# Kernel optimization log

Measured on AMD Instinct MI355X. Metric: run time of the kernel, lower is better.

Reference implementation:

```python
import jax, jax.numpy as jnp
import numpy as np
from jax import lax

# config (matches init_kwargs)
HEADS = 4
KD2 = 256          # key_dim // 2
KNN = 16
BLOCK = 128        # knn * block_rate
COL = 512          # value_size // block
VALUE_SIZE = 65536 # key_num ** 2
D_OUT = 512
D_IN = 1024
QUERYDIM = HEADS * KD2  # 1024
KERNEL = 3


def setup_inputs() -> dict:
    key = jax.random.key(0)
    ks = jax.random.split(key, 8)
    B, T = 2, 2048
    return {
        "x": jax.random.normal(ks[0], (B, T, D_IN), dtype=jnp.float32),
        "conv_w": jax.random.normal(ks[1], (D_IN, 1, KERNEL), dtype=jnp.float32) * 0.1,
        "conv_b": jax.random.normal(ks[2], (D_IN,), dtype=jnp.float32) * 0.1,
        "lin_w": jax.random.normal(ks[3], (QUERYDIM, D_IN), dtype=jnp.float32) * (D_IN ** -0.5),
        "lin_b": jax.random.normal(ks[4], (QUERYDIM,), dtype=jnp.float32) * 0.1,
        "rowkeys": jax.random.normal(ks[5], (BLOCK, HEADS, KD2), dtype=jnp.float32) * (KD2 ** -0.5),
        "colkeys": jax.random.normal(ks[6], (COL, HEADS, KD2), dtype=jnp.float32) * (KD2 ** -0.5),
        "value_w": jax.random.normal(ks[7], (VALUE_SIZE, D_OUT), dtype=jnp.float32),
    }


def _forward(x, conv_w, conv_b, lin_w, lin_b, rowkeys, colkeys, value_w):
    B, T, C = x.shape
    # --- Querynet: causal depthwise conv1d + linear ---
    xt = jnp.transpose(x, (0, 2, 1))  # (B, C, T)
    y = lax.conv_general_dilated(
        xt, conv_w, window_strides=(1,), padding=[(KERNEL - 1, 0)],
        feature_group_count=C, dimension_numbers=("NCH", "OIH", "NCH"))
    y = y + conv_b[None, :, None]
    y = jnp.transpose(y, (0, 2, 1))                     # (B, T, C)
    query = y @ lin_w.T + lin_b                         # (B, T, querydim)
    # torch: query.view(B, heads, T, key_dim//2) -- raw C-order reshape
    q = query.reshape(B, HEADS, T, KD2)
    # --- block_wise_choice.get_indices ---
    score = jnp.einsum("bhtd,ehd->bhte", q, rowkeys)    # (B,H,T,block)
    col_scores = jnp.einsum("bhtd,chd->bhtc", q, colkeys)  # (B,H,T,col)
    score_col, idx_col = lax.top_k(col_scores, 1)       # (B,H,T,1)
    base = jnp.arange(BLOCK, dtype=jnp.int32)
    indices = base[None, None, None, :] * COL + idx_col  # (B,H,T,block)
    score = score + score_col                            # broadcast add
    # torch .view(B,H,-1,T): raw C-order reshape mixing tokens and blocks
    score = score.reshape(B, HEADS, BLOCK, T)
    indices = indices.reshape(B, HEADS, BLOCK, T)
    k = T * KNN // BLOCK
    score_top, dispatch = lax.top_k(score, k)            # (B,H,block,k), sorted desc
    idx_top = jnp.take_along_axis(indices, dispatch, axis=-1)
    score_r = score_top.reshape(B, BLOCK, -1)            # (B, block, H*k)
    idx_r = idx_top.reshape(B, BLOCK, -1)
    disp_r = dispatch.reshape(B, BLOCK, -1)
    # --- Memory_value: gather-weight-scatter ---
    gathered = value_w[idx_r]                            # (B, block, H*k, d)
    weighted = (gathered * score_r[..., None]).reshape(B, -1, D_OUT)
    flat_disp = disp_r.reshape(B, -1)                    # values in [0, T)
    out = jnp.zeros((B, T, D_OUT), dtype=weighted.dtype)
    out = out.at[jnp.arange(B)[:, None], flat_disp].add(weighted)
    return out


def reference(x, conv_w, conv_b, lin_w, lin_b, rowkeys, colkeys, value_w):
    return _forward(x, conv_w, conv_b, lin_w, lin_b, rowkeys, colkeys, value_w)
```

## Files before the change

kernel.cpp:

```cpp
#include <hip/hip_runtime.h>

constexpr int Bc   = 2;
constexpr int Tc   = 2048;
constexpr int Cc   = 1024;
constexpr int QDc  = 1024;
constexpr int Hc   = 4;
constexpr int KD2c = 256;
constexpr int BLKc = 128;
constexpr int COLc = 512;
constexpr int DOUTc= 512;
constexpr int KSELc= 256;
constexpr int NKEYS= BLKc + COLc;
constexpr int NBINS= Bc * Tc;
constexpr int NSEL = Bc * Hc * BLKc * KSELc;

typedef short bf16x8 __attribute__((ext_vector_type(8)));
typedef float f32x4  __attribute__((ext_vector_type(4)));

__device__ __forceinline__ unsigned short f2bf(float f) {
    unsigned u = __float_as_uint(f);
    u += 0x7FFFu + ((u >> 16) & 1u);
    return (unsigned short)(u >> 16);
}
__device__ __forceinline__ float bf2f(unsigned short h) {
    return __uint_as_float((unsigned)h << 16);
}
__device__ __forceinline__ void splitbf3(float f, unsigned short* h,
                                         unsigned short* m, unsigned short* l) {
    unsigned short hh = f2bf(f);
    float r1 = f - bf2f(hh);
    unsigned short mm = f2bf(r1);
    float r2 = r1 - bf2f(mm);
    *h = hh; *m = mm; *l = f2bf(r2);
}

__device__ __forceinline__ void gld_lds16(const void* g, void* l) {
    __builtin_amdgcn_global_load_lds(
        (const __attribute__((address_space(1))) unsigned int*)g,
        (__attribute__((address_space(3))) unsigned int*)l, 16, 0, 0);
}

__global__ __launch_bounds__(256) void conv_kernel(
    const float* __restrict__ x, const float* __restrict__ cw,
    const float* __restrict__ cb, unsigned short* __restrict__ y1,
    unsigned short* __restrict__ y2, unsigned short* __restrict__ y3)
{
    int idx = blockIdx.x * 256 + threadIdx.x;
    int c = idx & (Cc - 1);
    int t = (idx >> 10) & (Tc - 1);
    int b = idx >> 21;
    float w0 = cw[c*3+0], w1 = cw[c*3+1], w2 = cw[c*3+2];
    const float* xb = x + (size_t)b * Tc * Cc;
    float acc = cb[c] + w2 * xb[(size_t)t*Cc + c];
    if (t >= 1) acc += w1 * xb[(size_t)(t-1)*Cc + c];
    if (t >= 2) acc += w0 * xb[(size_t)(t-2)*Cc + c];
    splitbf3(acc, &y1[idx], &y2[idx], &y3[idx]);
}

__global__ __launch_bounds__(256) void convw_kernel(
    const float* __restrict__ w, unsigned short* __restrict__ w1,
    unsigned short* __restrict__ w2, unsigned short* __restrict__ w3)
{
    int idx = blockIdx.x * 256 + threadIdx.x;
    splitbf3(w[idx], &w1[idx], &w2[idx], &w3[idx]);
}

__global__ __launch_bounds__(256) void convkeys_kernel(
    const float* __restrict__ rowkeys, const float* __restrict__ colkeys,
    unsigned short* __restrict__ k1, unsigned short* __restrict__ k2,
    unsigned short* __restrict__ k3)
{
    int bid = blockIdx.x;
    int h = bid / NKEYS, n = bid % NKEYS;
    int k = threadIdx.x;
    float v = (n < BLKc) ? rowkeys[((size_t)n*Hc + h)*KD2c + k]
                         : colkeys[((size_t)(n-BLKc)*Hc + h)*KD2c + k];
    size_t o = ((size_t)h*NKEYS + n)*KD2c + k;
    splitbf3(v, &k1[o], &k2[o], &k3[o]);
}

__device__ __forceinline__ void mfma_gemm_tile(
    const unsigned short* __restrict__ A1g, const unsigned short* __restrict__ A2g,
    const unsigned short* __restrict__ A3g, int lda,
    const unsigned short* __restrict__ B1g, const unsigned short* __restrict__ B2g,
    const unsigned short* __restrict__ B3g, int ldb,
    int K, int m0, int n0, char* lds, f32x4 acc[4][4])
{
    const int tid  = threadIdx.x;
    const int wave = tid >> 6, lane = tid & 63;
    const int wr = wave >> 1, wc = wave & 1;
    const int g = lane >> 4, r16 = lane & 15;

    int aoff[4], boff[4];
    #pragma unroll
    for (int i = 0; i < 4; i++) {
        int ra = wr*64 + i*16 + r16;
        aoff[i] = ra*64 + ((g ^ ((ra>>1)&3)) << 4);
        int rb = wc*64 + i*16 + r16;
        boff[i] = rb*64 + ((g ^ ((rb>>1)&3)) << 4);
    }
    const int c0 = wave*64 + lane;
    const int c1 = 256 + c0;
    const int row0 = c0 >> 2, kg0 = ((c0 & 3) ^ ((row0>>1)&3)) * 8;
    const int row1 = c1 >> 2, kg1 = ((c1 & 3) ^ ((row1>>1)&3)) * 8;
    char* d0 = lds + wave*1024;
    char* d1 = lds + 4096 + wave*1024;

    for (int kc = 0; kc < K; kc += 32) {
        size_t a0 = (size_t)(m0+row0)*lda + kc + kg0;
        size_t a1s = (size_t)(m0+row1)*lda + kc + kg1;
        size_t b0 = (size_t)(n0+row0)*ldb + kc + kg0;
        size_t b1s = (size_t)(n0+row1)*ldb + kc + kg1;
        gld_lds16(A1g + a0,  d0);
        gld_lds16(A1g + a1s, d1);
        gld_lds16(A2g + a0,  d0 + 8192);
        gld_lds16(A2g + a1s, d1 + 8192);
        gld_lds16(A3g + a0,  d0 + 16384);
        gld_lds16(A3g + a1s, d1 + 16384);
        gld_lds16(B1g + b0,  d0 + 24576);
        gld_lds16(B1g + b1s, d1 + 24576);
        gld_lds16(B2g + b0,  d0 + 32768);
        gld_lds16(B2g + b1s, d1 + 32768);
        gld_lds16(B3g + b0,  d0 + 40960);
        gld_lds16(B3g + b1s, d1 + 40960);
        __syncthreads();

        bf16x8 a1[4], a2[4], a3[4], b1[4], b2[4], b3[4];
        #pragma unroll
        for (int i = 0; i < 4; i++) {
            a1[i] = *(const bf16x8*)(lds + aoff[i]);
            a2[i] = *(const bf16x8*)(lds +  8192 + aoff[i]);
            a3[i] = *(const bf16x8*)(lds + 16384 + aoff[i]);
            b1[i] = *(const bf16x8*)(lds + 24576 + boff[i]);
            b2[i] = *(const bf16x8*)(lds + 32768 + boff[i]);
            b3[i] = *(const bf16x8*)(lds + 40960 + boff[i]);
        }
        #pragma unroll
        for (int i = 0; i < 4; i++)
            #pragma unroll
            for (int j = 0; j < 4; j++) {
                acc[i][j] = __builtin_amdgcn_mfma_f32_16x16x32_bf16(a3[i], b1[j], acc[i][j], 0, 0, 0);
                acc[i][j] = __builtin_amdgcn_mfma_f32_16x16x32_bf16(a2[i], b2[j], acc[i][j], 0, 0, 0);
                acc[i][j] = __builtin_amdgcn_mfma_f32_16x16x32_bf16(a1[i], b3[j], acc[i][j], 0, 0, 0);
                acc[i][j] = __builtin_amdgcn_mfma_f32_16x16x32_bf16(a2[i], b1[j], acc[i][j], 0, 0, 0);
                acc[i][j] = __builtin_amdgcn_mfma_f32_16x16x32_bf16(a1[i], b2[j], acc[i][j], 0, 0, 0);
                acc[i][j] = __builtin_amdgcn_mfma_f32_16x16x32_bf16(a1[i], b1[j], acc[i][j], 0, 0, 0);
            }
        __syncthreads();
    }
}

__global__ __launch_bounds__(256) void qgemm_kernel(
    const unsigned short* __restrict__ y1, const unsigned short* __restrict__ y2,
    const unsigned short* __restrict__ y3,
    const unsigned short* __restrict__ w1, const unsigned short* __restrict__ w2,
    const unsigned short* __restrict__ w3,
    const float* __restrict__ bias,
    unsigned short* __restrict__ q1, unsigned short* __restrict__ q2,
    unsigned short* __restrict__ q3)
{
    __shared__ char lds[49152];
    int m0 = blockIdx.y * 128, n0 = blockIdx.x * 128;
    f32x4 acc[4][4];
    #pragma unroll
    for (int i = 0; i < 4; i++)
        #pragma unroll
        for (int j = 0; j < 4; j++) acc[i][j] = (f32x4)0.f;
    mfma_gemm_tile(y1, y2, y3, Cc, w1, w2, w3, Cc, Cc, m0, n0, lds, acc);

    const int lane = threadIdx.x & 63, wave = threadIdx.x >> 6;
    const int wr = wave >> 1, wc = wave & 1;
    const int g = lane >> 4, r16 = lane & 15;
    #pragma unroll
    for (int i = 0; i < 4; i++)
        #pragma unroll
        for (int j = 0; j < 4; j++)
            #pragma unroll
            for (int reg = 0; reg < 4; reg++) {
                int m = m0 + wr*64 + i*16 + g*4 + reg;
                int n = n0 + wc*64 + j*16 + r16;
                float v = acc[i][j][reg] + bias[n];
                size_t o = (size_t)m * QDc + n;
                splitbf3(v, &q1[o], &q2[o], &q3[o]);
            }
}

__global__ __launch_bounds__(256) void sgemm_kernel(
    const unsigned short* __restrict__ q1, const unsigned short* __restrict__ q2,
    const unsigned short* __restrict__ q3,
    const unsigned short* __restrict__ k1, const unsigned short* __restrict__ k2,
    const unsigned short* __restrict__ k3,
    float* __restrict__ Ctmp)
{
    __shared__ char lds[49152];
    int b4h = blockIdx.z;
    size_t qo = (size_t)b4h * (Tc * KD2c);
    size_t ko = (size_t)(b4h & 3) * (NKEYS * KD2c);
    int m0 = blockIdx.y * 128, n0 = blockIdx.x * 128;
    f32x4 acc[4][4];
    #pragma unroll
    for (int i = 0; i < 4; i++)
        #pragma unroll
        for (int j = 0; j < 4; j++) acc[i][j] = (f32x4)0.f;
    mfma_gemm_tile(q1+qo, q2+qo, q3+qo, KD2c, k1+ko, k2+ko, k3+ko, KD2c,
                   KD2c, m0, n0, lds, acc);

    const int lane = threadIdx.x & 63, wave = threadIdx.x >> 6;
    const int wr = wave >> 1, wc = wave & 1;
    const int g = lane >> 4, r16 = lane & 15;
    float* Cb = Ctmp + (size_t)b4h * Tc * NKEYS;
    #pragma unroll
    for (int i = 0; i < 4; i++)
        #pragma unroll
        for (int j = 0; j < 4; j++)
            #pragma unroll
            for (int reg = 0; reg < 4; reg++) {
                int m = m0 + wr*64 + i*16 + g*4 + reg;
                int n = n0 + wc*64 + j*16 + r16;
                Cb[(size_t)m * NKEYS + n] = acc[i][j][reg];
            }
}

__global__ __launch_bounds__(256) void colmax_kernel(
    const float* __restrict__ Ctmp, float* __restrict__ s, int* __restrict__ cidx)
{
    int rid = blockIdx.x * 4 + (threadIdx.x >> 6);
    int lane = threadIdx.x & 63;
    const float* row = Ctmp + (size_t)rid * NKEYS;
    float best = -3.4e38f; int bi = 0;
    #pragma unroll
    for (int i = 0; i < 8; i++) {
        int c = lane + i*64;
        float v = row[BLKc + c];
        if (v > best) { best = v; bi = c; }
    }
    #pragma unroll
    for (int off = 32; off > 0; off >>= 1) {
        float ov = __shfl_xor(best, off, 64);
        int   oi = __shfl_xor(bi,   off, 64);
        if (ov > best || (ov == best && oi < bi)) { best = ov; bi = oi; }
    }
    if (lane == 0) cidx[rid] = bi;
    #pragma unroll
    for (int e = lane; e < BLKc; e += 64)
        s[(size_t)rid*BLKc + e] = row[e] + best;
}

__global__ __launch_bounds__(256) void topk_kernel(
    const float* __restrict__ s, const int* __restrict__ cidx,
    int* __restrict__ tk_j, int* __restrict__ tk_vidx, float* __restrict__ tk_score)
{
    int wid  = (blockIdx.x << 2) + (threadIdx.x >> 6);
    int lane = threadIdx.x & 63;
    int batch = wid >> 7;
    int i = wid & 127;
    const float* srow = s + (size_t)batch * (Tc*BLKc) + (size_t)i * 2048;

    unsigned key[8][4];
    #pragma unroll
    for (int r = 0; r < 8; r++) {
        float4 v4 = *(const float4*)&srow[r*256 + lane*4];
        float vv[4] = {v4.x, v4.y, v4.z, v4.w};
        #pragma unroll
        for (int e = 0; e < 4; e++) {
            unsigned u = __float_as_uint(vv[e]);
            key[r][e] = (u >> 31) ? ~u : (u | 0x80000000u);
        }
    }

    unsigned lo = 0, hi = 0xFFFFFFFFu;
    while (lo < hi) {
        unsigned d = hi - lo;
        unsigned mid = lo + ((d >> 1) + (d & 1u));
        int cnt = 0;
        #pragma unroll
        for (int r = 0; r < 8; r++)
            #pragma unroll
            for (int e = 0; e < 4; e++)
                cnt += (key[r][e] >= mid) ? 1 : 0;
        #pragma unroll
        for (int off = 32; off > 0; off >>= 1) cnt += __shfl_xor(cnt, off, 64);
        if (cnt >= KSELc) lo = mid; else hi = mid - 1;
    }
    const unsigned thr = lo;

    int gcnt = 0, ecnt = 0;
    unsigned eqmask = 0;
    #pragma unroll
    for (int r = 0; r < 8; r++)
        #pragma unroll
        for (int e = 0; e < 4; e++) {
            gcnt += (key[r][e] > thr) ? 1 : 0;
            if (key[r][e] == thr) { eqmask |= (1u << (r*4+e)); ecnt++; }
        }

    int gpre = gcnt, epre = ecnt;
    #pragma unroll
    for (int off = 1; off < 64; off <<= 1) {
        int gv = __shfl_up(gpre, off, 64);
        int ev = __shfl_up(epre, off, 64);
        if (lane >= off) { gpre += gv; epre += ev; }
    }
    const int total_greater = __shfl(gpre, 63, 64);
    const int total_eq      = __shfl(epre, 63, 64);
    const int gbase = gpre - gcnt;
    const int ebase = epre - ecnt;
    const int need  = KSELc - total_greater;

    const size_t obase = (size_t)wid * KSELc;
    const int cbase = batch * Tc + i * 16;

    int rk = 0;
    #pragma unroll
    for (int r = 0; r < 8; r++)
        #pragma unroll
        for (int e = 0; e < 4; e++) {
            if (key[r][e] > thr) {
                int j = r*256 + lane*4 + e;
                unsigned u = key[r][e];
                float f = (u >> 31) ? __uint_as_float(u ^ 0x80000000u)
                                    : __uint_as_float(~u);
                size_t o = obase + gbase + rk;
                tk_j[o] = j;
                tk_vidx[o] = (j & 127) * COLc + cidx[cbase + (j >> 7)];
                tk_score[o] = f;
                rk++;
            }
        }

    if (need == total_eq) {
        int erk = 0;
        #pragma unroll
        for (int r = 0; r < 8; r++)
            #pragma unroll
            for (int e = 0; e < 4; e++) {
                if (key[r][e] == thr) {
                    int j = r*256 + lane*4 + e;
                    float f = (thr >> 31) ? __uint_as_float(thr ^ 0x80000000u)
                                          : __uint_as_float(~thr);
                    size_t o = obase + total_greater + ebase + erk;
                    tk_j[o] = j;
                    tk_vidx[o] = (j & 127) * COLc + cidx[cbase + (j >> 7)];
                    tk_score[o] = f;
                    erk++;
                }
            }
    } else {
        unsigned em = eqmask;
        int left = need;
        while (left > 0) {
            int myj = 0x7FFFFFFF;
            if (em) {
                int bit = __builtin_ctz(em);
                myj = (bit >> 2)*256 + lane*4 + (bit & 3);
            }
            int mn = myj;
            #pragma unroll
            for (int off = 32; off > 0; off >>= 1) mn = min(mn, __shfl_xor(mn, off, 64));
            if (myj == mn) {
                em &= em - 1;
                int j = mn;
                float f = (thr >> 31) ? __uint_as_float(thr ^ 0x80000000u)
                                      : __uint_as_float(~thr);
                size_t o = obase + (KSELc - left);
                tk_j[o] = j;
                tk_vidx[o] = (j & 127) * COLc + cidx[cbase + (j >> 7)];
                tk_score[o] = f;
            }
            left--;
        }
    }
}

__global__ __launch_bounds__(256) void zero_bins_kernel(int* __restrict__ p, int n)
{
    int i = blockIdx.x * 256 + threadIdx.x;
    if (i < n) p[i] = 0;
}

__global__ __launch_bounds__(256) void count_kernel(
    const int* __restrict__ tk_j, int* __restrict__ counts)
{
    int idx = blockIdx.x * 256 + threadIdx.x;
    int r = idx >> 8;
    int b = r >> 9;
    int j = tk_j[idx];
    atomicAdd(&counts[b * Tc + j], 1);
}

__global__ __launch_bounds__(256) void scan_kernel(
    const int* __restrict__ counts, int* __restrict__ offsets)
{
    __shared__ int part[256];
    int tid = threadIdx.x;
    int local[16];
    int sum = 0;
    #pragma unroll
    for (int k = 0; k < 16; k++) { local[k] = sum; sum += counts[tid*16 + k]; }
    part[tid] = sum;
    __syncthreads();
    for (int st = 1; st < 256; st <<= 1) {
        int v = (tid >= st) ? part[tid - st] : 0;
        __syncthreads();
        part[tid] += v;
        __syncthreads();
    }
    int base = (tid == 0) ? 0 : part[tid - 1];
    #pragma unroll
    for (int k = 0; k < 16; k++) offsets[tid*16 + k] = base + local[k];
    if (tid == 255) offsets[NBINS] = base + sum;
}

__global__ __launch_bounds__(256) void fill_kernel(
    const int* __restrict__ tk_j, const int* __restrict__ tk_vidx,
    const float* __restrict__ tk_score, const int* __restrict__ offsets,
    int* __restrict__ fillctr, int* __restrict__ bin_vidx,
    float* __restrict__ bin_score)
{
    int idx = blockIdx.x * 256 + threadIdx.x;
    int r = idx >> 8;
    int b = r >> 9;
    int bin = b * Tc + tk_j[idx];
    int pos = offsets[bin] + atomicAdd(&fillctr[bin], 1);
    bin_vidx[pos]  = tk_vidx[idx];
    bin_score[pos] = tk_score[idx];
}

__global__ __launch_bounds__(256) void gather_kernel(
    const int* __restrict__ offsets, const int* __restrict__ bin_vidx,
    const float* __restrict__ bin_score, const float* __restrict__ value_w,
    float* __restrict__ out)
{
    __shared__ int   svidx[512];
    __shared__ float sscore[512];
    int bin = blockIdx.x;
    int tid = threadIdx.x;
    int beg = offsets[bin], cnt = offsets[bin + 1] - beg;
    for (int n = tid; n < cnt; n += 256) {
        svidx[n]  = bin_vidx[beg + n];
        sscore[n] = bin_score[beg + n];
    }
    __syncthreads();

    const int c = tid * 2;
    float accx = 0.f, accy = 0.f;
    int n = 0;
    for (; n + 4 <= cnt; n += 4) {
        int   v0 = svidx[n],    v1 = svidx[n+1],  v2 = svidx[n+2],  v3 = svidx[n+3];
        float s0 = sscore[n],   s1 = sscore[n+1], s2 = sscore[n+2], s3 = sscore[n+3];
        float2 a = *(const float2*)&value_w[(size_t)v0 * DOUTc + c];
        float2 b = *(const float2*)&value_w[(size_t)v1 * DOUTc + c];
        float2 d = *(const float2*)&value_w[(size_t)v2 * DOUTc + c];
        float2 e = *(const float2*)&value_w[(size_t)v3 * DOUTc + c];
        accx += s0*a.x; accy += s0*a.y;
        accx += s1*b.x; accy += s1*b.y;
        accx += s2*d.x; accy += s2*d.y;
        accx += s3*e.x; accy += s3*e.y;
    }
    for (; n < cnt; n++) {
        int v = svidx[n]; float sc = sscore[n];
        float2 a = *(const float2*)&value_w[(size_t)v * DOUTc + c];
        accx += sc*a.x; accy += sc*a.y;
    }
    float2 res; res.x = accx; res.y = accy;
    *(float2*)&out[(size_t)bin * DOUTc + c] = res;
}

extern "C" void kernel_launch(void* const* d_in, const int* in_sizes, int n_in,
                              void* d_out, int out_size, void* d_ws, size_t ws_size,
                              hipStream_t stream)
{
    const float* x       = (const float*)d_in[0];
    const float* conv_w  = (const float*)d_in[1];
    const float* conv_b  = (const float*)d_in[2];
    const float* lin_w   = (const float*)d_in[3];
    const float* lin_b   = (const float*)d_in[4];
    const float* rowkeys = (const float*)d_in[5];
    const float* colkeys = (const float*)d_in[6];
    const float* value_w = (const float*)d_in[7];
    float* out = (float*)d_out;

    constexpr size_t MB = 1024*1024;
    char* w = (char*)d_ws;
    float*          Ctmp = (float*)(w);
    unsigned short* y1   = (unsigned short*)(w);
    unsigned short* y2   = (unsigned short*)(w +  8*MB);
    unsigned short* y3   = (unsigned short*)(w + 16*MB);
    unsigned short* w1   = (unsigned short*)(w + 24*MB);
    unsigned short* w2   = (unsigned short*)(w + 26*MB);
    unsigned short* w3   = (unsigned short*)(w + 28*MB);
    unsigned short* q1   = (unsigned short*)(w + 40*MB);
    unsigned short* q2   = (unsigned short*)(w + 48*MB);
    unsigned short* q3   = (unsigned short*)(w + 56*MB);
    unsigned short* k1   = (unsigned short*)(w + 64*MB);
    unsigned short* k2   = (unsigned short*)(w + 66*MB);
    unsigned short* k3   = (unsigned short*)(w + 68*MB);
    float*          s    = (float*)(w + 70*MB);
    int*            cidx = (int*)  (w + 78*MB);
    int*            tk_j = (int*)  (w + 79*MB);
    int*            tk_v = (int*)  (w + 80*MB);
    float*          tk_s = (float*)(w + 81*MB);
    int*            counts    = (int*)  (w + 82*MB);
    int*            offsets   = (int*)  (w + 82*MB + 32768);
    int*            fillctr   = (int*)  (w + 82*MB + 65536);
    int*            bin_vidx  = (int*)  (w + 82*MB + 131072);
    float*          bin_score = (float*)(w + 82*MB + 131072 + 1048576);

    conv_kernel<<<(Bc*Tc*Cc)/256, 256, 0, stream>>>(x, conv_w, conv_b, y1, y2, y3);
    convw_kernel<<<(QDc*Cc)/256, 256, 0, stream>>>(lin_w, w1, w2, w3);
    convkeys_kernel<<<Hc*NKEYS, 256, 0, stream>>>(rowkeys, colkeys, k1, k2, k3);
    qgemm_kernel<<<dim3(QDc/128, (Bc*Tc)/128), 256, 0, stream>>>(
        y1, y2, y3, w1, w2, w3, lin_b, q1, q2, q3);
    sgemm_kernel<<<dim3(NKEYS/128, Tc/128, Bc*Hc), 256, 0, stream>>>(
        q1, q2, q3, k1, k2, k3, Ctmp);
    colmax_kernel<<<(Bc*Hc*Tc)/4, 256, 0, stream>>>(Ctmp, s, cidx);
    topk_kernel<<<Bc*Hc*BLKc/4, 256, 0, stream>>>(s, cidx, tk_j, tk_v, tk_s);
    zero_bins_kernel<<<(96*1024/4 + 255)/256, 256, 0, stream>>>(counts, 96*1024/4);
    count_kernel<<<NSEL/256, 256, 0, stream>>>(tk_j, counts);
    scan_kernel<<<1, 256, 0, stream>>>(counts, offsets);
    fill_kernel<<<NSEL/256, 256, 0, stream>>>(tk_j, tk_v, tk_s, offsets,
                                              fillctr, bin_vidx, bin_score);
    gather_kernel<<<NBINS, 256, 0, stream>>>(offsets, bin_vidx, bin_score,
                                             value_w, out);
}
```

Baseline: 278.3 us.

## Double-buffer LDS in the split-bf16 MFMA GEMM tile to overlap loads

```diff
diff --git a/kernel.cpp b/kernel.cpp
--- a/kernel.cpp
+++ b/kernel.cpp
@@ -106,34 +106,35 @@
     char* d0 = lds + wave*1024;
     char* d1 = lds + 4096 + wave*1024;
 
-    for (int kc = 0; kc < K; kc += 32) {
-        size_t a0 = (size_t)(m0+row0)*lda + kc + kg0;
-        size_t a1s = (size_t)(m0+row1)*lda + kc + kg1;
-        size_t b0 = (size_t)(n0+row0)*ldb + kc + kg0;
-        size_t b1s = (size_t)(n0+row1)*ldb + kc + kg1;
-        gld_lds16(A1g + a0,  d0);
-        gld_lds16(A1g + a1s, d1);
-        gld_lds16(A2g + a0,  d0 + 8192);
-        gld_lds16(A2g + a1s, d1 + 8192);
-        gld_lds16(A3g + a0,  d0 + 16384);
-        gld_lds16(A3g + a1s, d1 + 16384);
-        gld_lds16(B1g + b0,  d0 + 24576);
-        gld_lds16(B1g + b1s, d1 + 24576);
-        gld_lds16(B2g + b0,  d0 + 32768);
-        gld_lds16(B2g + b1s, d1 + 32768);
-        gld_lds16(B3g + b0,  d0 + 40960);
-        gld_lds16(B3g + b1s, d1 + 40960);
-        __syncthreads();
-
+#define STAGE(kc, bo) do {                                                 \
+        size_t a0_ = (size_t)(m0+row0)*lda + (kc) + kg0;                   \
+        size_t a1_ = (size_t)(m0+row1)*lda + (kc) + kg1;                   \
+        size_t b0_ = (size_t)(n0+row0)*ldb + (kc) + kg0;                   \
+        size_t b1_ = (size_t)(n0+row1)*ldb + (kc) + kg1;                   \
+        gld_lds16(A1g + a0_, d0 + (bo));                                   \
+        gld_lds16(A1g + a1_, d1 + (bo));                                   \
+        gld_lds16(A2g + a0_, d0 + 8192 + (bo));                            \
+        gld_lds16(A2g + a1_, d1 + 8192 + (bo));                            \
+        gld_lds16(A3g + a0_, d0 + 16384 + (bo));                           \
+        gld_lds16(A3g + a1_, d1 + 16384 + (bo));                           \
+        gld_lds16(B1g + b0_, d0 + 24576 + (bo));                           \
+        gld_lds16(B1g + b1_, d1 + 24576 + (bo));                           \
+        gld_lds16(B2g + b0_, d0 + 32768 + (bo));                           \
+        gld_lds16(B2g + b1_, d1 + 32768 + (bo));                           \
+        gld_lds16(B3g + b0_, d0 + 40960 + (bo));                           \
+        gld_lds16(B3g + b1_, d1 + 40960 + (bo));                           \
+    } while (0)
+
+    auto compute = [&](int bo) {
         bf16x8 a1[4], a2[4], a3[4], b1[4], b2[4], b3[4];
         #pragma unroll
         for (int i = 0; i < 4; i++) {
-            a1[i] = *(const bf16x8*)(lds + aoff[i]);
-            a2[i] = *(const bf16x8*)(lds +  8192 + aoff[i]);
-            a3[i] = *(const bf16x8*)(lds + 16384 + aoff[i]);
-            b1[i] = *(const bf16x8*)(lds + 24576 + boff[i]);
-            b2[i] = *(const bf16x8*)(lds + 32768 + boff[i]);
-            b3[i] = *(const bf16x8*)(lds + 40960 + boff[i]);
+            a1[i] = *(const bf16x8*)(lds + bo + aoff[i]);
+            a2[i] = *(const bf16x8*)(lds + bo +  8192 + aoff[i]);
+            a3[i] = *(const bf16x8*)(lds + bo + 16384 + aoff[i]);
+            b1[i] = *(const bf16x8*)(lds + bo + 24576 + boff[i]);
+            b2[i] = *(const bf16x8*)(lds + bo + 32768 + boff[i]);
+            b3[i] = *(const bf16x8*)(lds + bo + 40960 + boff[i]);
         }
         #pragma unroll
         for (int i = 0; i < 4; i++)
@@ -146,8 +147,26 @@
                 acc[i][j] = __builtin_amdgcn_mfma_f32_16x16x32_bf16(a1[i], b2[j], acc[i][j], 0, 0, 0);
                 acc[i][j] = __builtin_amdgcn_mfma_f32_16x16x32_bf16(a1[i], b1[j], acc[i][j], 0, 0, 0);
             }
-        __syncthreads();
-    }
+    };
+
+    const int NT = K / 32;
+    STAGE(0, 0);
+    int bo = 0;
+    for (int t = 0; t < NT - 1; ++t) {
+        STAGE((t+1)*32, bo ^ 49152);
+        asm volatile("s_waitcnt vmcnt(12)" ::: "memory");
+        __builtin_amdgcn_s_barrier();
+        asm volatile("" ::: "memory");
+        compute(bo);
+        asm volatile("" ::: "memory");
+        __builtin_amdgcn_s_barrier();
+        bo ^= 49152;
+    }
+    asm volatile("s_waitcnt vmcnt(0)" ::: "memory");
+    __builtin_amdgcn_s_barrier();
+    asm volatile("" ::: "memory");
+    compute(bo);
+#undef STAGE
 }
 
 __global__ __launch_bounds__(256) void qgemm_kernel(
@@ -159,7 +178,7 @@
     unsigned short* __restrict__ q1, unsigned short* __restrict__ q2,
     unsigned short* __restrict__ q3)
 {
-    __shared__ char lds[49152];
+    __shared__ char lds[98304];
     int m0 = blockIdx.y * 128, n0 = blockIdx.x * 128;
     f32x4 acc[4][4];
     #pragma unroll
@@ -192,7 +211,7 @@
     const unsigned short* __restrict__ k3,
     float* __restrict__ Ctmp)
 {
-    __shared__ char lds[49152];
+    __shared__ char lds[98304];
     int b4h = blockIdx.z;
     size_t qo = (size_t)b4h * (Tc * KD2c);
     size_t ko = (size_t)(b4h & 3) * (NKEYS * KD2c);
```

Measured after the change: 255.1 us. -8.3%, faster.
